# Optimization experiments

Hardware: AMD Instinct MI355X
Metric: run time of the kernel (lower is better)

The kernel has to match this reference:

```python
import jax, jax.numpy as jnp
import numpy as np

HIDDEN = 1024
N_HEAD = 16
LN_EPS = 1e-5


def _layernorm(x, g, b):
    m = jnp.mean(x, axis=-1, keepdims=True)
    v = jnp.var(x, axis=-1, keepdims=True)
    return (x - m) * jax.lax.rsqrt(v + LN_EPS) * g + b


def setup_inputs() -> dict:
    key = jax.random.key(0)
    ks = jax.random.split(key, 16)
    H = HIDDEN
    s = 0.02
    d = dict(
        x=jax.random.normal(ks[0], (4, 1024, H), jnp.float32),
        Wq=jax.random.normal(ks[1], (H, H), jnp.float32) * s,
        bq=jnp.zeros((H,), jnp.float32),
        Wk=jax.random.normal(ks[2], (H, H), jnp.float32) * s,
        bk=jnp.zeros((H,), jnp.float32),
        Wv=jax.random.normal(ks[3], (H, H), jnp.float32) * s,
        bv=jnp.zeros((H,), jnp.float32),
        Wo=jax.random.normal(ks[4], (H, H), jnp.float32) * s,
        bo=jnp.zeros((H,), jnp.float32),
        g1=jax.random.normal(ks[5], (H,), jnp.float32) * s,
        b1=jnp.zeros((H,), jnp.float32),
        W1=jax.random.normal(ks[6], (H, 4 * H), jnp.float32) * s,
        c1=jnp.zeros((4 * H,), jnp.float32),
        W2=jax.random.normal(ks[7], (4 * H, H), jnp.float32) * s,
        c2=jnp.zeros((H,), jnp.float32),
        g2=jax.random.normal(ks[8], (H,), jnp.float32) * s,
        b2=jnp.zeros((H,), jnp.float32),
    )
    return d


def reference(x, Wq, bq, Wk, bk, Wv, bv, Wo, bo, g1, b1, W1, c1, W2, c2, g2, b2):
    N, T, Hd = x.shape
    Hh = N_HEAD
    D = Hd // Hh
    # faithful to torch code: .view(N, H, T, D) is a raw reshape, no transpose
    q = (x @ Wq + bq).reshape(N, Hh, T, D)
    k = (x @ Wk + bk).reshape(N, Hh, T, D)
    v = (x @ Wv + bv).reshape(N, Hh, T, D)
    scores = jnp.einsum('nhtd,nhsd->nhts', q, k) / jnp.sqrt(jnp.float32(Hd))
    # faithful: softmax over dim=1 (the head axis)
    attn = jax.nn.softmax(scores, axis=1)
    o = jnp.einsum('nhts,nhsd->nhtd', attn, v).reshape(N, T, Hd)
    o = o @ Wo + bo
    x1 = _layernorm(o + x, g1, b1)
    ff = jax.nn.gelu(x1 @ W1 + c1, approximate=False) @ W2 + c2
    return _layernorm(ff + x1, g2, b2)
```

## Files before the change

### kernel.cpp

```cpp
#include <hip/hip_runtime.h>
#include <cstdint>
#include <cstddef>

#define EPI_QKV  0
#define EPI_F32  2
#define EPI_GELU 3
#define EPI_PART 4

typedef __attribute__((ext_vector_type(8))) short bfrag8;
typedef __attribute__((ext_vector_type(4))) float facc4;

struct PtrQuad { unsigned short* p[4]; };

__device__ __forceinline__ unsigned short f2b(float x) {
  unsigned int u = __builtin_bit_cast(unsigned int, x);
  u += 0x7FFFu + ((u >> 16) & 1u);
  return (unsigned short)(u >> 16);
}
__device__ __forceinline__ float b2f(unsigned short u) {
  unsigned int x = ((unsigned int)u) << 16;
  return __builtin_bit_cast(float, x);
}

__device__ __forceinline__ void gl2lds16(const unsigned short* g, unsigned short* l) {
  __builtin_amdgcn_global_load_lds(
      (const __attribute__((address_space(1))) unsigned int*)g,
      (__attribute__((address_space(3))) unsigned int*)l, 16, 0, 0);
}

__global__ __launch_bounds__(256)
void cvt_bf16_kernel(const float* __restrict__ in, unsigned short* __restrict__ out, int n4) {
  const int i = blockIdx.x * 256 + threadIdx.x;
  if (i < n4) {
    const float4 v = ((const float4*)in)[i];
    ushort4 u;
    u.x = f2b(v.x); u.y = f2b(v.y); u.z = f2b(v.z); u.w = f2b(v.w);
    ((ushort4*)out)[i] = u;
  }
}

__global__ __launch_bounds__(256)
void transpose_cvt(const float* __restrict__ in, unsigned short* __restrict__ out,
                   int K, int N) {
  __shared__ float tile[32][33];
  const int n0 = blockIdx.x * 32;
  const int k0 = blockIdx.y * 32;
  const int tx = threadIdx.x & 31, ty = threadIdx.x >> 5;
#pragma unroll
  for (int i = 0; i < 32; i += 8)
    tile[ty + i][tx] = in[(size_t)(k0 + ty + i) * N + n0 + tx];
  __syncthreads();
#pragma unroll
  for (int i = 0; i < 32; i += 8)
    out[(size_t)(n0 + ty + i) * K + k0 + tx] = f2b(tile[tx][ty + i]);
}

template<int EPI>
__global__ __launch_bounds__(256, 2)
void gemm_bt(const unsigned short* __restrict__ A,
             const unsigned short* __restrict__ Bt,
             const float* __restrict__ bias,
             const float* __restrict__ bias2,
             const float* __restrict__ bias3,
             void* __restrict__ out, PtrQuad pq,
             int M, int N, int K, int ldk) {
  __shared__ unsigned short sA[128 * 32];
  __shared__ unsigned short sB[128 * 32];
  const int tid  = threadIdx.x;
  const int lane = tid & 63;
  const int wave = tid >> 6;
  const int l15  = lane & 15, l4 = lane >> 4;
  const int wr = wave >> 1, wc = wave & 1;
  const long row0 = (long)blockIdx.y * 128;
  const long col0 = (long)blockIdx.x * 128;
  const long k0   = (long)blockIdx.z * K;

  facc4 acc[4][4];
#pragma unroll
  for (int i = 0; i < 4; i++)
#pragma unroll
    for (int j = 0; j < 4; j++) acc[i][j] = (facc4)0.f;

  const int srow = tid >> 2;
  const int scol = (tid & 3) * 8;
  const unsigned short* Ap0 = A  + (row0 + srow) * (long)ldk + k0 + scol;
  const unsigned short* Ap1 = Ap0 + 64 * (long)ldk;
  const unsigned short* Bp0 = Bt + (col0 + srow) * (long)ldk + k0 + scol;
  const unsigned short* Bp1 = Bp0 + 64 * (long)ldk;
  const int wbase = (tid & ~63) * 8;
  unsigned short* sA0 = &sA[wbase];
  unsigned short* sA1 = &sA[2048 + wbase];
  unsigned short* sB0 = &sB[wbase];
  unsigned short* sB1 = &sB[2048 + wbase];

  const int aoff = (wr * 64 + l15) * 32 + l4 * 8;
  const int boff = (wc * 64 + l15) * 32 + l4 * 8;

  for (int kt = 0; kt < K; kt += 32) {
    gl2lds16(Ap0 + kt, sA0);
    gl2lds16(Ap1 + kt, sA1);
    gl2lds16(Bp0 + kt, sB0);
    gl2lds16(Bp1 + kt, sB1);
    __syncthreads();
    bfrag8 af[4], bf[4];
#pragma unroll
    for (int i = 0; i < 4; i++) af[i] = *(const bfrag8*)&sA[aoff + i * 512];
#pragma unroll
    for (int j = 0; j < 4; j++) bf[j] = *(const bfrag8*)&sB[boff + j * 512];
#pragma unroll
    for (int i = 0; i < 4; i++)
#pragma unroll
      for (int j = 0; j < 4; j++)
        acc[i][j] = __builtin_amdgcn_mfma_f32_16x16x32_bf16(af[i], bf[j], acc[i][j], 0, 0, 0);
    __syncthreads();
  }

#pragma unroll
  for (int i = 0; i < 4; i++) {
    const long m0 = row0 + wr * 64 + i * 16 + l4 * 4;
#pragma unroll
    for (int j = 0; j < 4; j++) {
      const long c = col0 + wc * 64 + j * 16 + l15;
      if constexpr (EPI == EPI_QKV) {
        const long which = c >> 10;
        const long cl = c & 1023;
        unsigned short* oq = (unsigned short*)out;
        if (which == 0) {
          const float bj = bias[cl];
#pragma unroll
          for (int r = 0; r < 4; r++)
            oq[(m0 + r) * 1024 + cl] = f2b((acc[i][j][r] + bj) * 0.03125f);
        } else if (which == 1) {
          const float bj = bias2[cl];
#pragma unroll
          for (int r = 0; r < 4; r++)
            (oq + 4194304)[(m0 + r) * 1024 + cl] = f2b(acc[i][j][r] + bj);
        } else {
          const float bj = bias3[cl];
          const long cc = cl >> 6, d = cl & 63;
#pragma unroll
          for (int r = 0; r < 4; r++) {
            const long m = m0 + r;
            const long nbb = m >> 10, rr = m & 1023;
            const long h = rr >> 6, rhi = rr & 63;
            const long s = rhi * 16 + cc;
            (oq + 8388608)[((nbb * 16 + h) * 64 + d) * 1024 + s] = f2b(acc[i][j][r] + bj);
          }
        }
      } else if constexpr (EPI == EPI_F32) {
        const float bj = bias[c];
        float* of = (float*)out;
#pragma unroll
        for (int r = 0; r < 4; r++) of[(m0 + r) * (long)N + c] = acc[i][j][r] + bj;
      } else if constexpr (EPI == EPI_PART) {
        unsigned short* ob = pq.p[blockIdx.z];
#pragma unroll
        for (int r = 0; r < 4; r++) ob[(m0 + r) * (long)N + c] = f2b(acc[i][j][r]);
      } else {
        const float bj = bias[c];
        unsigned short* ob = (unsigned short*)out;
#pragma unroll
        for (int r = 0; r < 4; r++) {
          const float t = acc[i][j][r] + bj;
          ob[(m0 + r) * (long)N + c] = f2b(0.5f * t * (1.f + erff(t * 0.70710678f)));
        }
      }
    }
  }
}

__global__ __launch_bounds__(512, 4)
void attn_kernel(const unsigned short* __restrict__ Qb,
                 const unsigned short* __restrict__ Kb,
                 const unsigned short* __restrict__ Vt,
                 unsigned short* __restrict__ P0, unsigned short* __restrict__ P1) {
  const int id = blockIdx.x;
  const int combo = id & 7;
  const int tile = id >> 3;
  const int nb = combo & 3;
  const int sp = combo >> 2;
  const int tid = threadIdx.x, lane = tid & 63;
  const int w = __builtin_amdgcn_readfirstlane(tid >> 6);
  const int l15 = lane & 15, l4 = lane >> 4;
  const int t0 = tile * 16;

  __shared__ float red[2][8][576];
  __shared__ __align__(16) unsigned short abuf[8][16][40];

  const size_t hb0 = (size_t)(nb * 16 + w * 2) << 16;
  const unsigned short* qB = Qb + hb0;
  const unsigned short* kB = Kb + hb0;
  const unsigned short* vB = Vt + hb0;

  bfrag8 qf[2][2];
#pragma unroll
  for (int hh = 0; hh < 2; hh++)
#pragma unroll
    for (int ks = 0; ks < 2; ks++)
      qf[hh][ks] = *(const bfrag8*)(qB + (hh << 16) + (t0 + l15) * 64 + ks * 32 + l4 * 8);

  facc4 oacc[2][4];
#pragma unroll
  for (int hh = 0; hh < 2; hh++)
#pragma unroll
    for (int nt = 0; nt < 4; nt++) oacc[hh][nt] = (facc4)0.f;

  for (int it = 0; it < 16; ++it) {
    const int s0 = sp * 512 + it * 32;
    const int pb = it & 1;
    facc4 sacc[2][2];
#pragma unroll
    for (int hh = 0; hh < 2; hh++)
#pragma unroll
      for (int nt = 0; nt < 2; nt++) sacc[hh][nt] = (facc4)0.f;
#pragma unroll
    for (int hh = 0; hh < 2; hh++) {
      const unsigned short* kh = kB + (hh << 16);
#pragma unroll
      for (int ks = 0; ks < 2; ks++)
#pragma unroll
        for (int nt = 0; nt < 2; nt++) {
          const bfrag8 kf = *(const bfrag8*)(kh + (s0 + nt * 16 + l15) * 64 + ks * 32 + l4 * 8);
          sacc[hh][nt] = __builtin_amdgcn_mfma_f32_16x16x32_bf16(qf[hh][ks], kf, sacc[hh][nt], 0, 0, 0);
        }
    }
    bfrag8 vf0[4], vf1[4];
#pragma unroll
    for (int nt = 0; nt < 4; nt++) {
      vf0[nt] = *(const bfrag8*)(vB + (size_t)(nt * 16 + l15) * 1024 + s0 + l4 * 8);
      vf1[nt] = *(const bfrag8*)(vB + (1 << 16) + (size_t)(nt * 16 + l15) * 1024 + s0 + l4 * 8);
    }
#pragma unroll
    for (int nt = 0; nt < 2; nt++)
#pragma unroll
      for (int r = 0; r < 4; r++) {
        const float e0 = __expf(sacc[0][nt][r]);
        const float e1 = __expf(sacc[1][nt][r]);
        sacc[0][nt][r] = e0; sacc[1][nt][r] = e1;
        red[pb][w][(l4 * 4 + r) * 36 + nt * 16 + l15] = e0 + e1;
      }
    __syncthreads();
    float rinv[2][4];
#pragma unroll
    for (int nt = 0; nt < 2; nt++)
#pragma unroll
      for (int r = 0; r < 4; r++) {
        const int o = (l4 * 4 + r) * 36 + nt * 16 + l15;
        float s = 0.f;
#pragma unroll
        for (int ww = 0; ww < 8; ww++) s += red[pb][ww][o];
        rinv[nt][r] = 1.f / s;
      }
#pragma unroll
    for (int nt = 0; nt < 2; nt++)
#pragma unroll
      for (int r = 0; r < 4; r++)
        abuf[w][l4 * 4 + r][nt * 16 + l15] = f2b(sacc[0][nt][r] * rinv[nt][r]);
    {
      const bfrag8 af0 = *(const bfrag8*)&abuf[w][l15][l4 * 8];
#pragma unroll
      for (int nt = 0; nt < 4; nt++)
        oacc[0][nt] = __builtin_amdgcn_mfma_f32_16x16x32_bf16(af0, vf0[nt], oacc[0][nt], 0, 0, 0);
    }
#pragma unroll
    for (int nt = 0; nt < 2; nt++)
#pragma unroll
      for (int r = 0; r < 4; r++)
        abuf[w][l4 * 4 + r][nt * 16 + l15] = f2b(sacc[1][nt][r] * rinv[nt][r]);
    {
      const bfrag8 af1 = *(const bfrag8*)&abuf[w][l15][l4 * 8];
#pragma unroll
      for (int nt = 0; nt < 4; nt++)
        oacc[1][nt] = __builtin_amdgcn_mfma_f32_16x16x32_bf16(af1, vf1[nt], oacc[1][nt], 0, 0, 0);
    }
  }
  unsigned short* P = sp ? P1 : P0;
#pragma unroll
  for (int hh = 0; hh < 2; hh++) {
    const size_t rb = ((size_t)nb * 1024 + (size_t)(w * 2 + hh) * 64 + tile) * 1024;
#pragma unroll
    for (int nt = 0; nt < 4; nt++)
#pragma unroll
      for (int r = 0; r < 4; r++)
        P[rb + (size_t)(l4 * 4 + r) * 64 + nt * 16 + l15] = f2b(oacc[hh][nt][r]);
  }
}

__global__ __launch_bounds__(256)
void reduce_o2(const unsigned short* __restrict__ P0, const unsigned short* __restrict__ P1,
               unsigned short* __restrict__ OB, int n4) {
  const int i = blockIdx.x * 256 + threadIdx.x;
  if (i < n4) {
    const ushort4 a = ((const ushort4*)P0)[i];
    const ushort4 b = ((const ushort4*)P1)[i];
    ushort4 u;
    u.x = f2b(b2f(a.x) + b2f(b.x));
    u.y = f2b(b2f(a.y) + b2f(b.y));
    u.z = f2b(b2f(a.z) + b2f(b.z));
    u.w = f2b(b2f(a.w) + b2f(b.w));
    ((ushort4*)OB)[i] = u;
  }
}

__global__ __launch_bounds__(256)
void ln_red(const unsigned short* __restrict__ P0, const unsigned short* __restrict__ P1,
            const unsigned short* __restrict__ P2, const unsigned short* __restrict__ P3,
            const float* __restrict__ bias, const float* __restrict__ resid,
            const float* __restrict__ g, const float* __restrict__ be,
            float* __restrict__ outf, unsigned short* __restrict__ outb) {
  const int row = blockIdx.x, tid = threadIdx.x;
  const size_t o4 = (size_t)row * 256 + tid;
  const ushort4 a = ((const ushort4*)P0)[o4];
  const ushort4 b = ((const ushort4*)P1)[o4];
  const ushort4 c = ((const ushort4*)P2)[o4];
  const ushort4 d = ((const ushort4*)P3)[o4];
  const float4 vb = ((const float4*)bias)[tid];
  const float4 vr = ((const float4*)resid)[o4];
  float t0 = b2f(a.x) + b2f(b.x) + b2f(c.x) + b2f(d.x) + vb.x + vr.x;
  float t1 = b2f(a.y) + b2f(b.y) + b2f(c.y) + b2f(d.y) + vb.y + vr.y;
  float t2 = b2f(a.z) + b2f(b.z) + b2f(c.z) + b2f(d.z) + vb.z + vr.z;
  float t3 = b2f(a.w) + b2f(b.w) + b2f(c.w) + b2f(d.w) + vb.w + vr.w;
  float s = t0 + t1 + t2 + t3;
  float q = t0 * t0 + t1 * t1 + t2 * t2 + t3 * t3;
#pragma unroll
  for (int off = 32; off > 0; off >>= 1) {
    s += __shfl_down(s, off, 64);
    q += __shfl_down(q, off, 64);
  }
  __shared__ float rs_[4], rq_[4];
  if ((tid & 63) == 0) { rs_[tid >> 6] = s; rq_[tid >> 6] = q; }
  __syncthreads();
  const float S = rs_[0] + rs_[1] + rs_[2] + rs_[3];
  const float Q = rq_[0] + rq_[1] + rq_[2] + rq_[3];
  const float mean = S * (1.f / 1024.f);
  const float var  = Q * (1.f / 1024.f) - mean * mean;
  const float rstd = rsqrtf(var + 1e-5f);
  const float4 vg  = ((const float4*)g)[tid];
  const float4 vbe = ((const float4*)be)[tid];
  float o0 = (t0 - mean) * rstd * vg.x + vbe.x;
  float o1 = (t1 - mean) * rstd * vg.y + vbe.y;
  float o2 = (t2 - mean) * rstd * vg.z + vbe.z;
  float o3 = (t3 - mean) * rstd * vg.w + vbe.w;
  ((float4*)(outf + (size_t)row * 1024))[tid] = make_float4(o0, o1, o2, o3);
  if (outb != nullptr) {
    ushort4 u;
    u.x = f2b(o0); u.y = f2b(o1); u.z = f2b(o2); u.w = f2b(o3);
    ((ushort4*)(outb + (size_t)row * 1024))[tid] = u;
  }
}

extern "C" void kernel_launch(void* const* d_in, const int* in_sizes, int n_in,
                              void* d_out, int out_size, void* d_ws, size_t ws_size,
                              hipStream_t stream) {
  const float* x  = (const float*)d_in[0];
  const float* Wq = (const float*)d_in[1];
  const float* bq = (const float*)d_in[2];
  const float* Wk = (const float*)d_in[3];
  const float* bk = (const float*)d_in[4];
  const float* Wv = (const float*)d_in[5];
  const float* bv = (const float*)d_in[6];
  const float* Wo = (const float*)d_in[7];
  const float* bo = (const float*)d_in[8];
  const float* g1 = (const float*)d_in[9];
  const float* b1 = (const float*)d_in[10];
  const float* W1 = (const float*)d_in[11];
  const float* c1 = (const float*)d_in[12];
  const float* W2 = (const float*)d_in[13];
  const float* c2 = (const float*)d_in[14];
  const float* g2 = (const float*)d_in[15];
  const float* b2 = (const float*)d_in[16];
  float* out = (float*)d_out;

  char* ws = (char*)d_ws;
  unsigned short* XB  = (unsigned short*)(ws);
  unsigned short* WQT = (unsigned short*)(ws + 8388608);
  unsigned short* WKT = (unsigned short*)(ws + 10485760);
  unsigned short* WVT = (unsigned short*)(ws + 12582912);
  unsigned short* WOT = (unsigned short*)(ws + 14680064);
  unsigned short* W1T = (unsigned short*)(ws + 16777216);
  unsigned short* W2T = (unsigned short*)(ws + 25165824);
  float*          X1  = (float*)(ws + 33554432);
  unsigned short* X1B = (unsigned short*)(ws + 50331648);
  char* RB = ws + 58720256;
  unsigned short* QB  = (unsigned short*)(RB);
  unsigned short* KB  = (unsigned short*)(RB + 8388608);
  unsigned short* VT  = (unsigned short*)(RB + 16777216);
  unsigned short* OB  = (unsigned short*)(RB + 25165824);
  unsigned short* H1B = (unsigned short*)(RB);
  unsigned short* AP0 = (unsigned short*)(RB + 33554432);
  unsigned short* AP1 = (unsigned short*)(RB + 41943040);
  PtrQuad OPQ = { { QB, KB, VT, XB } };
  PtrQuad FPQ = { { XB, X1B, (unsigned short*)(RB + 33554432),
                    (unsigned short*)(RB + 41943040) } };
  PtrQuad ZQ = { { nullptr, nullptr, nullptr, nullptr } };

  const dim3 tb(256);
  cvt_bf16_kernel<<<dim3(4096), tb, 0, stream>>>(x, XB, 1048576);
  transpose_cvt<<<dim3(32, 32),  tb, 0, stream>>>(Wq, WQT, 1024, 1024);
  transpose_cvt<<<dim3(32, 32),  tb, 0, stream>>>(Wk, WKT, 1024, 1024);
  transpose_cvt<<<dim3(32, 32),  tb, 0, stream>>>(Wv, WVT, 1024, 1024);
  transpose_cvt<<<dim3(32, 32),  tb, 0, stream>>>(Wo, WOT, 1024, 1024);
  transpose_cvt<<<dim3(128, 32), tb, 0, stream>>>(W1, W1T, 1024, 4096);
  transpose_cvt<<<dim3(32, 128), tb, 0, stream>>>(W2, W2T, 4096, 1024);
  gemm_bt<EPI_QKV><<<dim3(24, 32), tb, 0, stream>>>(XB, WQT, bq, bk, bv, (void*)QB, ZQ,
                                                    4096, 3072, 1024, 1024);
  attn_kernel<<<dim3(512), dim3(512), 0, stream>>>(QB, KB, VT, AP0, AP1);
  reduce_o2<<<dim3(4096), tb, 0, stream>>>(AP0, AP1, OB, 1048576);
  gemm_bt<EPI_PART><<<dim3(8, 32, 4), tb, 0, stream>>>(OB, WOT, nullptr, nullptr, nullptr,
                                                       nullptr, OPQ, 4096, 1024, 256, 1024);
  ln_red<<<dim3(4096), tb, 0, stream>>>(QB, KB, VT, XB, bo, x, g1, b1, X1, X1B);
  gemm_bt<EPI_GELU><<<dim3(32, 32), tb, 0, stream>>>(X1B, W1T, c1, nullptr, nullptr,
                                                     (void*)H1B, ZQ, 4096, 4096, 1024, 1024);
  gemm_bt<EPI_PART><<<dim3(8, 32, 4), tb, 0, stream>>>(H1B, W2T, nullptr, nullptr, nullptr,
                                                       nullptr, FPQ, 4096, 1024, 1024, 4096);
  ln_red<<<dim3(4096), tb, 0, stream>>>(FPQ.p[0], FPQ.p[1], FPQ.p[2], FPQ.p[3], c2, X1,
                                        g2, b2, out, (unsigned short*)nullptr);
}
```

Before: 463.0 us.

## Restructure attention kernel with larger query tiles, LDS-staged swizzled Q, transposed score MFMA

The attention kernel now handles 32 query rows per block instead of 16 and 64 key positions per iteration instead of 32, halving the grid and the number of cross-warp reduction barriers. Q for all 16 heads is staged once into swizzled LDS, scores are computed as K·Q so each lane holds per-key values, and P is packed with v_cvt_pk_bf16_f32 into a swizzled per-warp buffer. The aim is to reuse K/V loads across twice as many query rows and reduce synchronization per key, at the cost of much more LDS and register pressure (launch bounds lowered to 1 block per CU) and fewer blocks in the grid.

Result: faster. 448.3 us (-3.2%).

```diff
diff --git a/kernel.cpp b/kernel.cpp
--- a/kernel.cpp
+++ b/kernel.cpp
@@ -169,120 +169,169 @@
   }
 }
 
-__global__ __launch_bounds__(512, 4)
+__global__ __launch_bounds__(512, 1)
 void attn_kernel(const unsigned short* __restrict__ Qb,
                  const unsigned short* __restrict__ Kb,
                  const unsigned short* __restrict__ Vt,
                  unsigned short* __restrict__ P0, unsigned short* __restrict__ P1) {
   const int id = blockIdx.x;
   const int combo = id & 7;
-  const int tile = id >> 3;
   const int nb = combo & 3;
   const int sp = combo >> 2;
+  const int tile = id >> 3;
   const int tid = threadIdx.x, lane = tid & 63;
   const int w = __builtin_amdgcn_readfirstlane(tid >> 6);
   const int l15 = lane & 15, l4 = lane >> 4;
-  const int t0 = tile * 16;
-
-  __shared__ float red[2][8][576];
-  __shared__ __align__(16) unsigned short abuf[8][16][40];
-
-  const size_t hb0 = (size_t)(nb * 16 + w * 2) << 16;
-  const unsigned short* qB = Qb + hb0;
-  const unsigned short* kB = Kb + hb0;
-  const unsigned short* vB = Vt + hb0;
-
-  bfrag8 qf[2][2];
+  const int t0 = tile * 32;
+  const int sbase = sp * 512;
+  const int h0 = w * 2;
+
+  __shared__ __align__(16) unsigned short Qs[16 * 32 * 64];
+  __shared__ float Ds[8][64][33];
+  __shared__ __align__(16) unsigned short Pw[8][1024];
+
+  const size_t bb = ((size_t)(nb * 16)) << 16;
+  const unsigned short* qB = Qb + bb;
+  const unsigned short* kB = Kb + bb;
+  const unsigned short* vB = Vt + bb;
+
+#pragma unroll
+  for (int kk = 0; kk < 8; kk++) {
+    const int j = kk * 512 + tid;
+    const int h = j >> 8, t = (j >> 3) & 31, d8 = j & 7;
+    const int4 v = *(const int4*)(qB + ((size_t)h << 16) + (size_t)(t0 + t) * 64 + d8 * 8);
+    *(int4*)((char*)Qs + h * 4096 + t * 128 + ((d8 * 16) ^ ((t & 7) << 4))) = v;
+  }
+
+  const int swz = (l15 & 7) << 4;
+  char* pw = (char*)&Pw[w][0];
+  const int pwrow = l15 * 128;
+
+  facc4 oacc[2][2][4];
 #pragma unroll
   for (int hh = 0; hh < 2; hh++)
 #pragma unroll
-    for (int ks = 0; ks < 2; ks++)
-      qf[hh][ks] = *(const bfrag8*)(qB + (hh << 16) + (t0 + l15) * 64 + ks * 32 + l4 * 8);
-
-  facc4 oacc[2][4];
-#pragma unroll
-  for (int hh = 0; hh < 2; hh++)
-#pragma unroll
-    for (int nt = 0; nt < 4; nt++) oacc[hh][nt] = (facc4)0.f;
-
-  for (int it = 0; it < 16; ++it) {
-    const int s0 = sp * 512 + it * 32;
-    const int pb = it & 1;
-    facc4 sacc[2][2];
+    for (int ts = 0; ts < 2; ts++)
+#pragma unroll
+      for (int nt = 0; nt < 4; nt++) oacc[hh][ts][nt] = (facc4)0.f;
+
+  __syncthreads();
+
+  for (int it = 0; it < 8; ++it) {
+    const int s0 = sbase + it * 64;
+    bfrag8 kf[2][4][2];
+#pragma unroll
+    for (int hh = 0; hh < 2; hh++) {
+      const unsigned short* kh_ = kB + ((size_t)(h0 + hh) << 16) + (size_t)l15 * 64 + l4 * 8;
+#pragma unroll
+      for (int ss = 0; ss < 4; ss++)
+#pragma unroll
+        for (int kh = 0; kh < 2; kh++)
+          kf[hh][ss][kh] = *(const bfrag8*)(kh_ + (size_t)(s0 + ss * 16) * 64 + kh * 32);
+    }
+    bfrag8 vf[2][2][4];
+#pragma unroll
+    for (int hh = 0; hh < 2; hh++) {
+      const unsigned short* vh_ = vB + ((size_t)(h0 + hh) << 16) + (size_t)l15 * 1024 + s0 + l4 * 8;
+#pragma unroll
+      for (int sk = 0; sk < 2; sk++)
+#pragma unroll
+        for (int nt = 0; nt < 4; nt++)
+          vf[hh][sk][nt] = *(const bfrag8*)(vh_ + (size_t)(nt * 16) * 1024 + sk * 32);
+    }
+    facc4 sc[2][2][4];
 #pragma unroll
     for (int hh = 0; hh < 2; hh++)
 #pragma unroll
-      for (int nt = 0; nt < 2; nt++) sacc[hh][nt] = (facc4)0.f;
-#pragma unroll
-    for (int hh = 0; hh < 2; hh++) {
-      const unsigned short* kh = kB + (hh << 16);
-#pragma unroll
-      for (int ks = 0; ks < 2; ks++)
-#pragma unroll
-        for (int nt = 0; nt < 2; nt++) {
-          const bfrag8 kf = *(const bfrag8*)(kh + (s0 + nt * 16 + l15) * 64 + ks * 32 + l4 * 8);
-          sacc[hh][nt] = __builtin_amdgcn_mfma_f32_16x16x32_bf16(qf[hh][ks], kf, sacc[hh][nt], 0, 0, 0);
-        }
-    }
-    bfrag8 vf0[4], vf1[4];
-#pragma unroll
-    for (int nt = 0; nt < 4; nt++) {
-      vf0[nt] = *(const bfrag8*)(vB + (size_t)(nt * 16 + l15) * 1024 + s0 + l4 * 8);
-      vf1[nt] = *(const bfrag8*)(vB + (1 << 16) + (size_t)(nt * 16 + l15) * 1024 + s0 + l4 * 8);
-    }
-#pragma unroll
-    for (int nt = 0; nt < 2; nt++)
-#pragma unroll
-      for (int r = 0; r < 4; r++) {
-        const float e0 = __expf(sacc[0][nt][r]);
-        const float e1 = __expf(sacc[1][nt][r]);
-        sacc[0][nt][r] = e0; sacc[1][nt][r] = e1;
-        red[pb][w][(l4 * 4 + r) * 36 + nt * 16 + l15] = e0 + e1;
+      for (int ts = 0; ts < 2; ts++) {
+        const char* qh = (const char*)Qs + (h0 + hh) * 4096 + (ts * 16 + l15) * 128;
+        const bfrag8 q0 = *(const bfrag8*)(qh + ((l4 * 16) ^ swz));
+        const bfrag8 q1 = *(const bfrag8*)(qh + ((64 + l4 * 16) ^ swz));
+#pragma unroll
+        for (int ss = 0; ss < 4; ss++) {
+          facc4 a = __builtin_amdgcn_mfma_f32_16x16x32_bf16(kf[hh][ss][0], q0, (facc4)0.f, 0, 0, 0);
+          sc[hh][ts][ss] = __builtin_amdgcn_mfma_f32_16x16x32_bf16(kf[hh][ss][1], q1, a, 0, 0, 0);
+        }
+      }
+    facc4 dacc[2][4];
+#pragma unroll
+    for (int ts = 0; ts < 2; ts++)
+#pragma unroll
+      for (int ss = 0; ss < 4; ss++) dacc[ts][ss] = (facc4)0.f;
+#pragma unroll
+    for (int hh = 0; hh < 2; hh++)
+#pragma unroll
+      for (int ts = 0; ts < 2; ts++)
+#pragma unroll
+        for (int ss = 0; ss < 4; ss++)
+#pragma unroll
+          for (int r = 0; r < 4; r++) {
+            const float e = __expf(sc[hh][ts][ss][r]);
+            sc[hh][ts][ss][r] = e;
+            dacc[ts][ss][r] += e;
+          }
+#pragma unroll
+    for (int ts = 0; ts < 2; ts++)
+#pragma unroll
+      for (int ss = 0; ss < 4; ss++)
+#pragma unroll
+        for (int r = 0; r < 4; r++)
+          Ds[w][ss * 16 + l4 * 4 + r][ts * 16 + l15] = dacc[ts][ss][r];
+    __syncthreads();
+    facc4 rt[2][4];
+#pragma unroll
+    for (int ts = 0; ts < 2; ts++)
+#pragma unroll
+      for (int ss = 0; ss < 4; ss++)
+#pragma unroll
+        for (int r = 0; r < 4; r++) {
+          const int si = ss * 16 + l4 * 4 + r;
+          const int ti = ts * 16 + l15;
+          float s_ = Ds[0][si][ti];
+#pragma unroll
+          for (int ww = 1; ww < 8; ww++) s_ += Ds[ww][si][ti];
+          rt[ts][ss][r] = 1.f / s_;
+        }
+#pragma unroll
+    for (int hh = 0; hh < 2; hh++)
+#pragma unroll
+      for (int ts = 0; ts < 2; ts++) {
+#pragma unroll
+        for (int ss = 0; ss < 4; ss++) {
+          const float p0 = sc[hh][ts][ss][0] * rt[ts][ss][0];
+          const float p1 = sc[hh][ts][ss][1] * rt[ts][ss][1];
+          const float p2 = sc[hh][ts][ss][2] * rt[ts][ss][2];
+          const float p3 = sc[hh][ts][ss][3] * rt[ts][ss][3];
+          uint2 pk;
+          asm("v_cvt_pk_bf16_f32 %0, %1, %2" : "=v"(pk.x) : "v"(p0), "v"(p1));
+          asm("v_cvt_pk_bf16_f32 %0, %1, %2" : "=v"(pk.y) : "v"(p2), "v"(p3));
+          *(uint2*)(pw + pwrow + ((ss * 32 + l4 * 8) ^ swz)) = pk;
+        }
+        const bfrag8 a0 = *(const bfrag8*)(pw + pwrow + ((l4 * 16) ^ swz));
+        const bfrag8 a1 = *(const bfrag8*)(pw + pwrow + ((64 + l4 * 16) ^ swz));
+#pragma unroll
+        for (int nt = 0; nt < 4; nt++) {
+          oacc[hh][ts][nt] = __builtin_amdgcn_mfma_f32_16x16x32_bf16(a0, vf[hh][0][nt],
+                                                                    oacc[hh][ts][nt], 0, 0, 0);
+          oacc[hh][ts][nt] = __builtin_amdgcn_mfma_f32_16x16x32_bf16(a1, vf[hh][1][nt],
+                                                                    oacc[hh][ts][nt], 0, 0, 0);
+        }
       }
     __syncthreads();
-    float rinv[2][4];
-#pragma unroll
-    for (int nt = 0; nt < 2; nt++)
-#pragma unroll
-      for (int r = 0; r < 4; r++) {
-        const int o = (l4 * 4 + r) * 36 + nt * 16 + l15;
-        float s = 0.f;
-#pragma unroll
-        for (int ww = 0; ww < 8; ww++) s += red[pb][ww][o];
-        rinv[nt][r] = 1.f / s;
-      }
-#pragma unroll
-    for (int nt = 0; nt < 2; nt++)
-#pragma unroll
-      for (int r = 0; r < 4; r++)
-        abuf[w][l4 * 4 + r][nt * 16 + l15] = f2b(sacc[0][nt][r] * rinv[nt][r]);
-    {
-      const bfrag8 af0 = *(const bfrag8*)&abuf[w][l15][l4 * 8];
+  }
+
+  unsigned short* P = sp ? P1 : P0;
+#pragma unroll
+  for (int hh = 0; hh < 2; hh++) {
+    const size_t hb = ((size_t)nb << 20) + ((size_t)(h0 + hh) << 16);
+#pragma unroll
+    for (int ts = 0; ts < 2; ts++)
 #pragma unroll
       for (int nt = 0; nt < 4; nt++)
-        oacc[0][nt] = __builtin_amdgcn_mfma_f32_16x16x32_bf16(af0, vf0[nt], oacc[0][nt], 0, 0, 0);
-    }
-#pragma unroll
-    for (int nt = 0; nt < 2; nt++)
-#pragma unroll
-      for (int r = 0; r < 4; r++)
-        abuf[w][l4 * 4 + r][nt * 16 + l15] = f2b(sacc[1][nt][r] * rinv[nt][r]);
-    {
-      const bfrag8 af1 = *(const bfrag8*)&abuf[w][l15][l4 * 8];
-#pragma unroll
-      for (int nt = 0; nt < 4; nt++)
-        oacc[1][nt] = __builtin_amdgcn_mfma_f32_16x16x32_bf16(af1, vf1[nt], oacc[1][nt], 0, 0, 0);
-    }
-  }
-  unsigned short* P = sp ? P1 : P0;
-#pragma unroll
-  for (int hh = 0; hh < 2; hh++) {
-    const size_t rb = ((size_t)nb * 1024 + (size_t)(w * 2 + hh) * 64 + tile) * 1024;
-#pragma unroll
-    for (int nt = 0; nt < 4; nt++)
-#pragma unroll
-      for (int r = 0; r < 4; r++)
-        P[rb + (size_t)(l4 * 4 + r) * 64 + nt * 16 + l15] = f2b(oacc[hh][nt][r]);
+#pragma unroll
+        for (int r = 0; r < 4; r++)
+          P[hb + (size_t)(t0 + ts * 16 + l4 * 4 + r) * 64 + nt * 16 + l15] =
+              f2b(oacc[hh][ts][nt][r]);
   }
 }
 
@@ -404,7 +453,7 @@
   transpose_cvt<<<dim3(32, 128), tb, 0, stream>>>(W2, W2T, 4096, 1024);
   gemm_bt<EPI_QKV><<<dim3(24, 32), tb, 0, stream>>>(XB, WQT, bq, bk, bv, (void*)QB, ZQ,
                                                     4096, 3072, 1024, 1024);
-  attn_kernel<<<dim3(512), dim3(512), 0, stream>>>(QB, KB, VT, AP0, AP1);
+  attn_kernel<<<dim3(256), dim3(512), 0, stream>>>(QB, KB, VT, AP0, AP1);
   reduce_o2<<<dim3(4096), tb, 0, stream>>>(AP0, AP1, OB, 1048576);
   gemm_bt<EPI_PART><<<dim3(8, 32, 4), tb, 0, stream>>>(OB, WOT, nullptr, nullptr, nullptr,
                                                        nullptr, OPQ, 4096, 1024, 256, 1024);
```
